# Performance work log

Measured on AMD Instinct MI355X. Metric: run time of the kernel, lower is better.

Reference implementation:

```python
import jax, jax.numpy as jnp
import numpy as np

N = 50000      # nodes
E = 800000     # edges (before self-loops)
F_IN = 767     # input feature dim
HID = 256      # hidden = 8 heads * 32
NEG_SLOPE = 0.2


def setup_inputs() -> dict:
    key = jax.random.key(0)
    ks = jax.random.split(key, 10)
    x = jax.random.normal(ks[0], (N, F_IN), dtype=jnp.float32)
    edge_index = jax.random.randint(ks[1], (2, E), 0, N, dtype=jnp.int64)
    # GATConv 1: 767 -> 8 heads x 32 (concat -> 256)
    W1 = jax.random.normal(ks[2], (F_IN, HID), dtype=jnp.float32) * 0.05
    att_src1 = jax.random.normal(ks[3], (8, 32), dtype=jnp.float32) * 0.1
    att_dst1 = jax.random.normal(ks[4], (8, 32), dtype=jnp.float32) * 0.1
    b1 = jnp.zeros((HID,), dtype=jnp.float32)
    # GATConv 2: 256 -> 1 head x 10 (mean -> 10)
    W2 = jax.random.normal(ks[5], (HID, 10), dtype=jnp.float32) * 0.05
    att_src2 = jax.random.normal(ks[6], (1, 10), dtype=jnp.float32) * 0.1
    att_dst2 = jax.random.normal(ks[7], (1, 10), dtype=jnp.float32) * 0.1
    b2 = jnp.zeros((10,), dtype=jnp.float32)
    return {"x": x, "edge_index": edge_index, "W1": W1, "att_src1": att_src1,
            "att_dst1": att_dst1, "b1": b1, "W2": W2, "att_src2": att_src2,
            "att_dst2": att_dst2, "b2": b2}


def _gat_conv(x, src, dst, W, att_s, att_d, b, heads, ch, concat):
    """PyG GATConv (eval mode, dropout inactive). x:[N,Fin], src/dst:[E']."""
    n = x.shape[0]
    h = (x @ W).reshape(n, heads, ch)                      # [N,H,C]
    a_s = jnp.sum(h * att_s, axis=-1)                      # [N,H]
    a_d = jnp.sum(h * att_d, axis=-1)                      # [N,H]
    e = jax.nn.leaky_relu(a_s[src] + a_d[dst], NEG_SLOPE)  # [E',H]
    # destination-grouped (segment) softmax, numerically stable
    m = jax.lax.stop_gradient(jax.ops.segment_max(e, dst, num_segments=n))
    p = jnp.exp(e - m[dst])                                # [E',H]
    denom = jax.ops.segment_sum(p, dst, num_segments=n)    # [N,H]
    alpha = p / (denom[dst] + 1e-16)                       # [E',H]
    # scatter-aggregate weighted messages
    out = jax.ops.segment_sum(alpha[:, :, None] * h[src], dst, num_segments=n)
    out = out.reshape(n, heads * ch) if concat else out.mean(axis=1)
    return out + b


def reference(x, edge_index, W1, att_src1, att_dst1, b1, W2, att_src2, att_dst2, b2):
    n = x.shape[0]
    loops = jnp.arange(n, dtype=edge_index.dtype)
    src = jnp.concatenate([edge_index[0], loops])
    dst = jnp.concatenate([edge_index[1], loops])
    h = jax.nn.elu(_gat_conv(x, src, dst, W1, att_src1, att_dst1, b1, 8, 32, True))
    # dropout is a no-op in eval mode
    return _gat_conv(h, src, dst, W2, att_src2, att_dst2, b2, 1, 10, False)
```

## Files before the change

### kernel.cpp

```cpp
#include <hip/hip_runtime.h>
#include <hip/hip_fp16.h>

#define N_NODES 50000
#define N_EDGES 800000
#define EL (N_EDGES + N_NODES)
#define F_IN 767
#define HID 256
#define NHEAD 8
#define KSTEPS 24
#define NCH 12
#define NB_SCAN 49

typedef __attribute__((ext_vector_type(8))) short short8;
typedef __attribute__((ext_vector_type(4))) float f32x4;

struct H4 { __half2 a, b; };

static __device__ __forceinline__ unsigned short f2bf(float f) {
  unsigned int u = __float_as_uint(f);
  unsigned int r = (u + 0x7fffu + ((u >> 16) & 1u)) >> 16;
  return (unsigned short)r;
}
static __device__ __forceinline__ float bf2f(unsigned short h) {
  return __uint_as_float(((unsigned int)h) << 16);
}

__global__ __launch_bounds__(256) void prep_kernel(
    const float* __restrict__ W, short* __restrict__ Wh, short* __restrict__ Wl) {
  int idx = blockIdx.x * 256 + threadIdx.x;
  int k = idx >> 8, n = idx & 255;
  float v = (k < F_IN) ? W[k * HID + n] : 0.f;
  unsigned short h = f2bf(v);
  float lf = v - bf2f(h);
  unsigned short lo = f2bf(lf);
  int ks = k >> 5, oct = (k >> 3) & 3, j = k & 7;
  int nf = n >> 4;
  int l = (n & 15) | (oct << 4);
  int addr = ((ks * 16 + nf) * 64 + l) * 8 + j;
  Wh[addr] = (short)h;
  Wl[addr] = (short)lo;
}

__global__ __launch_bounds__(256, 2) void gemm1_mfma_kernel(
    const float* __restrict__ x, const short* __restrict__ Wh,
    const short* __restrict__ Wl, __half* __restrict__ h1h,
    const float* __restrict__ att_s, const float* __restrict__ att_d,
    float* __restrict__ as1, float* __restrict__ ad1) {
  __shared__ __align__(16) short Ah[2][2][2048];
  __shared__ __align__(16) short Al[2][2][2048];
  const int tid = threadIdx.x;
  const int lane = tid & 63, wav = tid >> 6;
  const int m0 = blockIdx.x * 64;
  const int m_local = tid >> 2, oct = tid & 3;
  const int gm = m0 + m_local;
  const bool vrow = (gm < N_NODES);
  const long xbase = (long)gm * F_IN;
  const int wu0 = ((m_local >> 4) * 64) + ((m_local & 15) | (oct << 4));
  const int wu = wu0 ^ ((((unsigned)wu0 >> 4) & 3) << 1);

  float atts[4], attd[4];
#pragma unroll
  for (int nf = 0; nf < 4; ++nf) {
    int c = wav * 64 + nf * 16 + (lane & 15);
    atts[nf] = att_s[c];
    attd[nf] = att_d[c];
  }

  f32x4 acc[4][4];
#pragma unroll
  for (int i = 0; i < 4; ++i)
#pragma unroll
    for (int j = 0; j < 4; ++j) acc[i][j] = (f32x4){0.f, 0.f, 0.f, 0.f};

  float xc[16], xn[16];
  {
    int kb = oct * 8;
    if (vrow) {
#pragma unroll
      for (int ki = 0; ki < 2; ++ki)
#pragma unroll
        for (int j = 0; j < 8; ++j) {
          xc[ki * 8 + j] = x[xbase + kb + ki * 32 + j];
          xn[ki * 8 + j] = x[xbase + 64 + kb + ki * 32 + j];
        }
    } else {
#pragma unroll
      for (int j = 0; j < 16; ++j) { xc[j] = 0.f; xn[j] = 0.f; }
    }
  }
  short8 bhc[4], blc[4];
  {
    const short* wb = Wh + ((wav * 4) * 64 + lane) * 8;
    const short* wbl = Wl + ((wav * 4) * 64 + lane) * 8;
#pragma unroll
    for (int nf = 0; nf < 4; ++nf) {
      bhc[nf] = *(const short8*)(wb + nf * 512);
      blc[nf] = *(const short8*)(wbl + nf * 512);
    }
  }

#pragma unroll 2
  for (int c = 0; c < NCH; ++c) {
#pragma unroll
    for (int ki = 0; ki < 2; ++ki) {
      short8 hi8, lo8;
#pragma unroll
      for (int j = 0; j < 8; ++j) {
        float v = xc[ki * 8 + j];
        unsigned short h = f2bf(v);
        hi8[j] = (short)h;
        lo8[j] = (short)f2bf(v - bf2f(h));
      }
      *(short8*)&Ah[c & 1][ki][wu * 8] = hi8;
      *(short8*)&Al[c & 1][ki][wu * 8] = lo8;
    }
    {
#pragma unroll
      for (int j = 0; j < 16; ++j) xc[j] = xn[j];
      int s = c + 2;
      if (s < NCH - 1) {
        int kb = s * 64 + oct * 8;
        if (vrow) {
#pragma unroll
          for (int ki = 0; ki < 2; ++ki)
#pragma unroll
            for (int j = 0; j < 8; ++j) xn[ki * 8 + j] = x[xbase + kb + ki * 32 + j];
        } else {
#pragma unroll
          for (int j = 0; j < 16; ++j) xn[j] = 0.f;
        }
      } else if (s == NCH - 1) {
        int kb = s * 64 + oct * 8;
#pragma unroll
        for (int ki = 0; ki < 2; ++ki)
#pragma unroll
          for (int j = 0; j < 8; ++j) {
            int k = kb + ki * 32 + j;
            xn[ki * 8 + j] = (vrow && k < F_IN) ? x[xbase + k] : 0.f;
          }
      }
    }
    __syncthreads();
#pragma unroll
    for (int ki = 0; ki < 2; ++ki) {
      const int ksg = c * 2 + ki;
      short8 ah[4], al[4];
#pragma unroll
      for (int mf = 0; mf < 4; ++mf) {
        int u = mf * 64 + lane;
        int us = u ^ ((((unsigned)u >> 4) & 3) << 1);
        ah[mf] = *(short8*)&Ah[c & 1][ki][us * 8];
        al[mf] = *(short8*)&Al[c & 1][ki][us * 8];
      }
      short8 bhn[4], bln[4];
      if (ksg + 1 < KSTEPS) {
        const short* wb = Wh + (((ksg + 1) * 16 + wav * 4) * 64 + lane) * 8;
        const short* wbl = Wl + (((ksg + 1) * 16 + wav * 4) * 64 + lane) * 8;
#pragma unroll
        for (int nf = 0; nf < 4; ++nf) {
          bhn[nf] = *(const short8*)(wb + nf * 512);
          bln[nf] = *(const short8*)(wbl + nf * 512);
        }
      }
#pragma unroll
      for (int mf = 0; mf < 4; ++mf)
#pragma unroll
        for (int nf = 0; nf < 4; ++nf)
          acc[mf][nf] = __builtin_amdgcn_mfma_f32_16x16x32_bf16(ah[mf], bhc[nf], acc[mf][nf], 0, 0, 0);
#pragma unroll
      for (int mf = 0; mf < 4; ++mf)
#pragma unroll
        for (int nf = 0; nf < 4; ++nf)
          acc[mf][nf] = __builtin_amdgcn_mfma_f32_16x16x32_bf16(ah[mf], blc[nf], acc[mf][nf], 0, 0, 0);
#pragma unroll
      for (int mf = 0; mf < 4; ++mf)
#pragma unroll
        for (int nf = 0; nf < 4; ++nf)
          acc[mf][nf] = __builtin_amdgcn_mfma_f32_16x16x32_bf16(al[mf], bhc[nf], acc[mf][nf], 0, 0, 0);
#pragma unroll
      for (int nf = 0; nf < 4; ++nf) {
        bhc[nf] = bhn[nf];
        blc[nf] = bln[nf];
      }
    }
  }

  const int r0 = (lane >> 4) * 4, cn = lane & 15;
#pragma unroll
  for (int mf = 0; mf < 4; ++mf) {
    int rowb = m0 + mf * 16 + r0;
#pragma unroll
    for (int rr = 0; rr < 4; ++rr) {
      int row = rowb + rr;
      bool ok = (row < N_NODES);
      if (ok) {
#pragma unroll
        for (int nf = 0; nf < 4; ++nf)
          h1h[(long)row * HID + wav * 64 + nf * 16 + cn] =
              __float2half_rn(acc[mf][nf][rr]);
      }
      float s0 = acc[mf][0][rr] * atts[0] + acc[mf][1][rr] * atts[1];
      float s1 = acc[mf][2][rr] * atts[2] + acc[mf][3][rr] * atts[3];
      float d0 = acc[mf][0][rr] * attd[0] + acc[mf][1][rr] * attd[1];
      float d1 = acc[mf][2][rr] * attd[2] + acc[mf][3][rr] * attd[3];
#pragma unroll
      for (int o = 1; o < 16; o <<= 1) {
        s0 += __shfl_xor(s0, o, 64);
        s1 += __shfl_xor(s1, o, 64);
        d0 += __shfl_xor(d0, o, 64);
        d1 += __shfl_xor(d1, o, 64);
      }
      if (ok && cn == 0) {
        as1[row * NHEAD + wav * 2]     = s0;
        as1[row * NHEAD + wav * 2 + 1] = s1;
        ad1[row * NHEAD + wav * 2]     = d0;
        ad1[row * NHEAD + wav * 2 + 1] = d1;
      }
    }
  }
}

__global__ void count_kernel(const int* __restrict__ ei, int* __restrict__ deg) {
  int e = blockIdx.x * blockDim.x + threadIdx.x;
  if (e >= EL) return;
  int dst = (e < N_EDGES) ? ei[N_EDGES + e] : (e - N_EDGES);
  atomicAdd(&deg[dst], 1);
}

__global__ __launch_bounds__(1024) void scan_part_kernel(
    const int* __restrict__ deg, int* __restrict__ off, int* __restrict__ btot) {
  __shared__ int warp_sums[16];
  const int tid = threadIdx.x;
  const int lane = tid & 63, wid = tid >> 6;
  int i = blockIdx.x * 1024 + tid;
  int v = (i < N_NODES) ? deg[i] : 0;
  int x = v;
#pragma unroll
  for (int o = 1; o < 64; o <<= 1) {
    int y = __shfl_up(x, o, 64);
    if (lane >= o) x += y;
  }
  if (lane == 63) warp_sums[wid] = x;
  __syncthreads();
  if (wid == 0) {
    int ws = (lane < 16) ? warp_sums[lane] : 0;
#pragma unroll
    for (int o = 1; o < 16; o <<= 1) {
      int y = __shfl_up(ws, o, 64);
      if (lane >= o) ws += y;
    }
    if (lane < 16) warp_sums[lane] = ws;
  }
  __syncthreads();
  int wprefix = (wid > 0) ? warp_sums[wid - 1] : 0;
  if (i < N_NODES) off[i] = wprefix + x - v;
  if (tid == 1023) btot[blockIdx.x] = warp_sums[15];
}

__global__ __launch_bounds__(64) void scan_tops_kernel(
    const int* __restrict__ btot, int* __restrict__ bo) {
  int lane = threadIdx.x;
  int v = (lane < NB_SCAN) ? btot[lane] : 0;
  int x = v;
#pragma unroll
  for (int o = 1; o < 64; o <<= 1) {
    int y = __shfl_up(x, o, 64);
    if (lane >= o) x += y;
  }
  if (lane < NB_SCAN) bo[lane] = x - v;
}

__global__ void scan_add_kernel(int* __restrict__ off, const int* __restrict__ bo) {
  int i = blockIdx.x * blockDim.x + threadIdx.x;
  if (i > N_NODES) return;
  if (i == N_NODES) off[i] = EL;
  else off[i] += bo[i >> 10];
}

__global__ void fill_p1_kernel(const int* __restrict__ ei, const int* __restrict__ off,
                               int* __restrict__ cur, const float* __restrict__ as1,
                               const float* __restrict__ ad1, int* __restrict__ csr,
                               float* __restrict__ p1) {
  int e = blockIdx.x * blockDim.x + threadIdx.x;
  if (e >= EL) return;
  int src, dst;
  if (e < N_EDGES) { src = ei[e]; dst = ei[N_EDGES + e]; }
  else { src = e - N_EDGES; dst = src; }
  int slot = off[dst] + atomicAdd(&cur[dst], 1);
  csr[slot] = src;
  float4 s0 = *(const float4*)&as1[src * NHEAD];
  float4 s1 = *(const float4*)&as1[src * NHEAD + 4];
  float4 d0 = *(const float4*)&ad1[dst * NHEAD];
  float4 d1 = *(const float4*)&ad1[dst * NHEAD + 4];
  float ev[8] = {s0.x + d0.x, s0.y + d0.y, s0.z + d0.z, s0.w + d0.w,
                 s1.x + d1.x, s1.y + d1.y, s1.z + d1.z, s1.w + d1.w};
  float pv[8];
#pragma unroll
  for (int h = 0; h < 8; ++h) {
    float t = ev[h];
    t = (t >= 0.f) ? t : 0.2f * t;
    pv[h] = __expf(t);
  }
  *(float4*)&p1[slot * 8]     = make_float4(pv[0], pv[1], pv[2], pv[3]);
  *(float4*)&p1[slot * 8 + 4] = make_float4(pv[4], pv[5], pv[6], pv[7]);
}

__global__ __launch_bounds__(256) void agg1_kernel(
    const __half* __restrict__ h1h, const float* __restrict__ p1,
    const int* __restrict__ off, const int* __restrict__ csr,
    const float* __restrict__ b1, const float* __restrict__ W2,
    const float* __restrict__ att_s2, const float* __restrict__ att_d2,
    float* __restrict__ h2, float* __restrict__ as2, float* __restrict__ ad2) {
  __shared__ float W2s[HID * 11];
  {
    int tid = threadIdx.x;
    for (int i = tid; i < HID * 10; i += 256)
      W2s[(i / 10) * 11 + (i % 10)] = W2[i];
  }
  __syncthreads();
  const int t = threadIdx.x & 63;
  const int n = blockIdx.x * 4 + (threadIdx.x >> 6);
  if (n >= N_NODES) return;
  const int head = t >> 3;
  const int j0 = off[n], j1 = off[n + 1];
  float a0 = 0.f, a1 = 0.f, a2 = 0.f, a3 = 0.f, den = 0.f;
  int j = j0;
  for (; j + 3 < j1; j += 4) {
    int s[4];
    float pw[4];
    H4 v[4];
#pragma unroll
    for (int q = 0; q < 4; ++q) s[q] = csr[j + q];
#pragma unroll
    for (int q = 0; q < 4; ++q) {
      pw[q] = p1[(j + q) * 8 + head];
      v[q] = *(const H4*)&h1h[s[q] * HID + t * 4];
    }
#pragma unroll
    for (int q = 0; q < 4; ++q) {
      float2 fa = __half22float2(v[q].a), fb = __half22float2(v[q].b);
      den += pw[q];
      a0 += pw[q] * fa.x;
      a1 += pw[q] * fa.y;
      a2 += pw[q] * fb.x;
      a3 += pw[q] * fb.y;
    }
  }
  for (; j < j1; ++j) {
    int s0 = csr[j];
    float p0 = p1[j * 8 + head];
    H4 v0 = *(const H4*)&h1h[s0 * HID + t * 4];
    float2 fa = __half22float2(v0.a), fb = __half22float2(v0.b);
    den += p0;
    a0 += p0 * fa.x;
    a1 += p0 * fa.y;
    a2 += p0 * fb.x;
    a3 += p0 * fb.y;
  }
  float rden = 1.f / (den + 1e-16f);
  float4 bv = *(const float4*)&b1[t * 4];
  float vv[4];
  vv[0] = a0 * rden + bv.x;
  vv[1] = a1 * rden + bv.y;
  vv[2] = a2 * rden + bv.z;
  vv[3] = a3 * rden + bv.w;
#pragma unroll
  for (int c = 0; c < 4; ++c) vv[c] = (vv[c] > 0.f) ? vv[c] : (__expf(vv[c]) - 1.f);
  float hk[10];
#pragma unroll
  for (int k = 0; k < 10; ++k) {
    float pk = vv[0] * W2s[(t * 4 + 0) * 11 + k] +
               vv[1] * W2s[(t * 4 + 1) * 11 + k] +
               vv[2] * W2s[(t * 4 + 2) * 11 + k] +
               vv[3] * W2s[(t * 4 + 3) * 11 + k];
#pragma unroll
    for (int o = 32; o >= 1; o >>= 1) pk += __shfl_xor(pk, o, 64);
    hk[k] = pk;
  }
  if (t == 0) {
    float s = 0.f, d = 0.f;
#pragma unroll
    for (int k = 0; k < 10; ++k) {
      h2[n * 10 + k] = hk[k];
      s += hk[k] * att_s2[k];
      d += hk[k] * att_d2[k];
    }
    as2[n] = s;
    ad2[n] = d;
  }
}

__global__ __launch_bounds__(256) void agg2_kernel(
    const float* __restrict__ h2, const float* __restrict__ as2,
    const float* __restrict__ ad2, const int* __restrict__ off,
    const int* __restrict__ csr, const float* __restrict__ b2,
    float* __restrict__ out) {
  int g = threadIdx.x >> 4, l = threadIdx.x & 15;
  int n = blockIdx.x * 16 + g;
  if (n >= N_NODES) return;
  float adn = ad2[n];
  int j0 = off[n], j1 = off[n + 1];
  float acc = 0.f, den = 0.f;
  int j = j0;
  for (; j + 1 < j1; j += 2) {
    int s0 = csr[j], s1 = csr[j + 1];
    float e0 = as2[s0] + adn, e1 = as2[s1] + adn;
    e0 = (e0 >= 0.f) ? e0 : 0.2f * e0;
    e1 = (e1 >= 0.f) ? e1 : 0.2f * e1;
    float p0 = __expf(e0), p1v = __expf(e1);
    den += p0 + p1v;
    if (l < 10) acc += p0 * h2[s0 * 10 + l] + p1v * h2[s1 * 10 + l];
  }
  if (j < j1) {
    int s0 = csr[j];
    float e0 = as2[s0] + adn;
    e0 = (e0 >= 0.f) ? e0 : 0.2f * e0;
    float p0 = __expf(e0);
    den += p0;
    if (l < 10) acc += p0 * h2[s0 * 10 + l];
  }
  if (l < 10) out[n * 10 + l] = acc / (den + 1e-16f) + b2[l];
}

extern "C" void kernel_launch(void* const* d_in, const int* in_sizes, int n_in,
                              void* d_out, int out_size, void* d_ws, size_t ws_size,
                              hipStream_t stream) {
  const float* x    = (const float*)d_in[0];
  const int*   ei   = (const int*)d_in[1];
  const float* W1   = (const float*)d_in[2];
  const float* as1w = (const float*)d_in[3];
  const float* ad1w = (const float*)d_in[4];
  const float* b1   = (const float*)d_in[5];
  const float* W2   = (const float*)d_in[6];
  const float* as2w = (const float*)d_in[7];
  const float* ad2w = (const float*)d_in[8];
  const float* b2   = (const float*)d_in[9];
  float* out = (float*)d_out;

  char* p = (char*)d_ws;
  __half* h1h = (__half*)p; p += (size_t)N_NODES * HID * 2;
  float* a_s1 = (float*)p; p += (size_t)N_NODES * NHEAD * 4;
  float* a_d1 = (float*)p; p += (size_t)N_NODES * NHEAD * 4;
  float* h2   = (float*)p; p += (size_t)N_NODES * 10 * 4;
  float* a_s2 = (float*)p; p += (size_t)N_NODES * 4;
  float* a_d2 = (float*)p; p += (size_t)N_NODES * 4;
  short* Wh   = (short*)p; p += (size_t)KSTEPS * 16 * 64 * 8 * 2;
  short* Wl   = (short*)p; p += (size_t)KSTEPS * 16 * 64 * 8 * 2;
  int* deg    = (int*)p;   p += (size_t)N_NODES * 4;
  int* cur    = (int*)p;   p += (size_t)N_NODES * 4;
  int* off    = (int*)p;   p += (size_t)(N_NODES + 1) * 4;
  int* csr    = (int*)p;   p += (size_t)EL * 4;
  float* p1   = (float*)p; p += (size_t)EL * NHEAD * 4;
  int* btot   = (int*)p;   p += 64 * 4;
  int* bo     = (int*)p;   p += 64 * 4;

  prep_kernel<<<768, 256, 0, stream>>>(W1, Wh, Wl);
  gemm1_mfma_kernel<<<(N_NODES + 63) / 64, 256, 0, stream>>>(
      x, Wh, Wl, h1h, as1w, ad1w, a_s1, a_d1);
  hipMemsetAsync(deg, 0, (size_t)N_NODES * 2 * 4, stream);
  count_kernel<<<(EL + 255) / 256, 256, 0, stream>>>(ei, deg);
  scan_part_kernel<<<NB_SCAN, 1024, 0, stream>>>(deg, off, btot);
  scan_tops_kernel<<<1, 64, 0, stream>>>(btot, bo);
  scan_add_kernel<<<(N_NODES + 256) / 256, 256, 0, stream>>>(off, bo);
  fill_p1_kernel<<<(EL + 255) / 256, 256, 0, stream>>>(ei, off, cur, a_s1, a_d1, csr, p1);
  agg1_kernel<<<(N_NODES + 3) / 4, 256, 0, stream>>>(
      h1h, p1, off, csr, b1, W2, as2w, ad2w, h2, a_s2, a_d2);
  agg2_kernel<<<(N_NODES + 15) / 16, 256, 0, stream>>>(h2, a_s2, a_d2, off, csr, b2, out);
}
```

Before: 290.9 us.

## Drop lo-split of x in GEMM and recompute edge weights in aggregation

The first GEMM no longer splits the input activations into hi/lo bf16 parts. It drops one of three MFMA passes and the matching LDS buffer, keeping the W hi/lo split. The per-edge exp weights are no longer precomputed into a slot-indexed buffer in the CSR fill kernel; agg1 recomputes them from the source and destination attention scores. This removes the p1 buffer's writes and reads at the cost of redundant exp work per lane, plus reduced GEMM precision (x rounded to bf16).

After: 282.5 us. -2.9%, faster.

```diff
diff --git a/kernel.cpp b/kernel.cpp
--- a/kernel.cpp
+++ b/kernel.cpp
@@ -47,7 +47,6 @@
     const float* __restrict__ att_s, const float* __restrict__ att_d,
     float* __restrict__ as1, float* __restrict__ ad1) {
   __shared__ __align__(16) short Ah[2][2][2048];
-  __shared__ __align__(16) short Al[2][2][2048];
   const int tid = threadIdx.x;
   const int lane = tid & 63, wav = tid >> 6;
   const int m0 = blockIdx.x * 64;
@@ -103,16 +102,10 @@
   for (int c = 0; c < NCH; ++c) {
 #pragma unroll
     for (int ki = 0; ki < 2; ++ki) {
-      short8 hi8, lo8;
-#pragma unroll
-      for (int j = 0; j < 8; ++j) {
-        float v = xc[ki * 8 + j];
-        unsigned short h = f2bf(v);
-        hi8[j] = (short)h;
-        lo8[j] = (short)f2bf(v - bf2f(h));
-      }
+      short8 hi8;
+#pragma unroll
+      for (int j = 0; j < 8; ++j) hi8[j] = (short)f2bf(xc[ki * 8 + j]);
       *(short8*)&Ah[c & 1][ki][wu * 8] = hi8;
-      *(short8*)&Al[c & 1][ki][wu * 8] = lo8;
     }
     {
 #pragma unroll
@@ -144,13 +137,12 @@
 #pragma unroll
     for (int ki = 0; ki < 2; ++ki) {
       const int ksg = c * 2 + ki;
-      short8 ah[4], al[4];
+      short8 ah[4];
 #pragma unroll
       for (int mf = 0; mf < 4; ++mf) {
         int u = mf * 64 + lane;
         int us = u ^ ((((unsigned)u >> 4) & 3) << 1);
         ah[mf] = *(short8*)&Ah[c & 1][ki][us * 8];
-        al[mf] = *(short8*)&Al[c & 1][ki][us * 8];
       }
       short8 bhn[4], bln[4];
       if (ksg + 1 < KSTEPS) {
@@ -172,11 +164,6 @@
 #pragma unroll
         for (int nf = 0; nf < 4; ++nf)
           acc[mf][nf] = __builtin_amdgcn_mfma_f32_16x16x32_bf16(ah[mf], blc[nf], acc[mf][nf], 0, 0, 0);
-#pragma unroll
-      for (int mf = 0; mf < 4; ++mf)
-#pragma unroll
-        for (int nf = 0; nf < 4; ++nf)
-          acc[mf][nf] = __builtin_amdgcn_mfma_f32_16x16x32_bf16(al[mf], bhc[nf], acc[mf][nf], 0, 0, 0);
 #pragma unroll
       for (int nf = 0; nf < 4; ++nf) {
         bhc[nf] = bhn[nf];
@@ -277,40 +264,24 @@
   else off[i] += bo[i >> 10];
 }
 
-__global__ void fill_p1_kernel(const int* __restrict__ ei, const int* __restrict__ off,
-                               int* __restrict__ cur, const float* __restrict__ as1,
-                               const float* __restrict__ ad1, int* __restrict__ csr,
-                               float* __restrict__ p1) {
+__global__ void fill_kernel(const int* __restrict__ ei, const int* __restrict__ off,
+                            int* __restrict__ cur, int* __restrict__ csr) {
   int e = blockIdx.x * blockDim.x + threadIdx.x;
   if (e >= EL) return;
   int src, dst;
   if (e < N_EDGES) { src = ei[e]; dst = ei[N_EDGES + e]; }
   else { src = e - N_EDGES; dst = src; }
-  int slot = off[dst] + atomicAdd(&cur[dst], 1);
-  csr[slot] = src;
-  float4 s0 = *(const float4*)&as1[src * NHEAD];
-  float4 s1 = *(const float4*)&as1[src * NHEAD + 4];
-  float4 d0 = *(const float4*)&ad1[dst * NHEAD];
-  float4 d1 = *(const float4*)&ad1[dst * NHEAD + 4];
-  float ev[8] = {s0.x + d0.x, s0.y + d0.y, s0.z + d0.z, s0.w + d0.w,
-                 s1.x + d1.x, s1.y + d1.y, s1.z + d1.z, s1.w + d1.w};
-  float pv[8];
-#pragma unroll
-  for (int h = 0; h < 8; ++h) {
-    float t = ev[h];
-    t = (t >= 0.f) ? t : 0.2f * t;
-    pv[h] = __expf(t);
-  }
-  *(float4*)&p1[slot * 8]     = make_float4(pv[0], pv[1], pv[2], pv[3]);
-  *(float4*)&p1[slot * 8 + 4] = make_float4(pv[4], pv[5], pv[6], pv[7]);
+  int pos = atomicAdd(&cur[dst], 1);
+  csr[off[dst] + pos] = src;
 }
 
 __global__ __launch_bounds__(256) void agg1_kernel(
-    const __half* __restrict__ h1h, const float* __restrict__ p1,
-    const int* __restrict__ off, const int* __restrict__ csr,
-    const float* __restrict__ b1, const float* __restrict__ W2,
-    const float* __restrict__ att_s2, const float* __restrict__ att_d2,
-    float* __restrict__ h2, float* __restrict__ as2, float* __restrict__ ad2) {
+    const __half* __restrict__ h1h, const float* __restrict__ as1,
+    const float* __restrict__ ad1, const int* __restrict__ off,
+    const int* __restrict__ csr, const float* __restrict__ b1,
+    const float* __restrict__ W2, const float* __restrict__ att_s2,
+    const float* __restrict__ att_d2, float* __restrict__ h2,
+    float* __restrict__ as2, float* __restrict__ ad2) {
   __shared__ float W2s[HID * 11];
   {
     int tid = threadIdx.x;
@@ -322,6 +293,7 @@
   const int n = blockIdx.x * 4 + (threadIdx.x >> 6);
   if (n >= N_NODES) return;
   const int head = t >> 3;
+  const float adn = ad1[n * NHEAD + head];
   const int j0 = off[n], j1 = off[n + 1];
   float a0 = 0.f, a1 = 0.f, a2 = 0.f, a3 = 0.f, den = 0.f;
   int j = j0;
@@ -333,7 +305,9 @@
     for (int q = 0; q < 4; ++q) s[q] = csr[j + q];
 #pragma unroll
     for (int q = 0; q < 4; ++q) {
-      pw[q] = p1[(j + q) * 8 + head];
+      float e = as1[s[q] * NHEAD + head] + adn;
+      e = (e >= 0.f) ? e : 0.2f * e;
+      pw[q] = __expf(e);
       v[q] = *(const H4*)&h1h[s[q] * HID + t * 4];
     }
 #pragma unroll
@@ -348,7 +322,9 @@
   }
   for (; j < j1; ++j) {
     int s0 = csr[j];
-    float p0 = p1[j * 8 + head];
+    float e = as1[s0 * NHEAD + head] + adn;
+    e = (e >= 0.f) ? e : 0.2f * e;
+    float p0 = __expf(e);
     H4 v0 = *(const H4*)&h1h[s0 * HID + t * 4];
     float2 fa = __half22float2(v0.a), fb = __half22float2(v0.b);
     den += p0;
@@ -450,7 +426,6 @@
   int* cur    = (int*)p;   p += (size_t)N_NODES * 4;
   int* off    = (int*)p;   p += (size_t)(N_NODES + 1) * 4;
   int* csr    = (int*)p;   p += (size_t)EL * 4;
-  float* p1   = (float*)p; p += (size_t)EL * NHEAD * 4;
   int* btot   = (int*)p;   p += 64 * 4;
   int* bo     = (int*)p;   p += 64 * 4;
 
@@ -462,8 +437,8 @@
   scan_part_kernel<<<NB_SCAN, 1024, 0, stream>>>(deg, off, btot);
   scan_tops_kernel<<<1, 64, 0, stream>>>(btot, bo);
   scan_add_kernel<<<(N_NODES + 256) / 256, 256, 0, stream>>>(off, bo);
-  fill_p1_kernel<<<(EL + 255) / 256, 256, 0, stream>>>(ei, off, cur, a_s1, a_d1, csr, p1);
+  fill_kernel<<<(EL + 255) / 256, 256, 0, stream>>>(ei, off, cur, csr);
   agg1_kernel<<<(N_NODES + 3) / 4, 256, 0, stream>>>(
-      h1h, p1, off, csr, b1, W2, as2w, ad2w, h2, a_s2, a_d2);
+      h1h, a_s1, a_d1, off, csr, b1, W2, as2w, ad2w, h2, a_s2, a_d2);
   agg2_kernel<<<(N_NODES + 15) / 16, 256, 0, stream>>>(h2, a_s2, a_d2, off, csr, b2, out);
 }
```
